# Optimization experiments

Measured on AMD Instinct MI355X. Metric: run time of the kernel, lower is better.

Reference implementation:

```python
import jax, jax.numpy as jnp
import numpy as np

K = 20  # kNN fan-out


def knn_idx(x, k):
    # x: (B, C, N). Negative squared pairwise distance; top-k largest = nearest.
    inner = -2.0 * jnp.einsum('bcn,bcm->bnm', x, x)        # (B, N, N)
    xx = jnp.sum(x * x, axis=1)                            # (B, N)
    pd = -xx[:, :, None] - inner - xx[:, None, :]          # (B, N, N)
    return jax.lax.top_k(pd, k)[1]                         # (B, N, k) int32


def get_graph_feature(x, k):
    # x: (B, C, N) -> edge features (B, 2C, N, k)
    idx = knn_idx(x, k)                                    # (B, N, k)
    xt = jnp.transpose(x, (0, 2, 1))                       # (B, N, C)
    nbrs = jax.vmap(lambda pts, ids: pts[ids])(xt, idx)    # (B, N, k, C)
    center = xt[:, :, None, :]                             # (B, N, 1, C)
    feat = jnp.concatenate(
        [nbrs - center, jnp.broadcast_to(center, nbrs.shape)], axis=-1)  # (B,N,k,2C)
    return jnp.transpose(feat, (0, 3, 1, 2))               # (B, 2C, N, k)


def vn_layer(W, x):
    # W: (out, in); x: (B, in, N, k) -> (B, out, N, k)
    return jnp.einsum('oi,bink->bonk', W, x)


def setup_inputs() -> dict:
    key = jax.random.key(0)
    ks = jax.random.split(key, 6)
    B, C, N = 16, 3, 2048
    num_classes = 10
    return {
        'x': jax.random.normal(ks[0], (B, C, N), dtype=jnp.float32),
        'W1': jax.random.normal(ks[1], (64, 6), dtype=jnp.float32),
        'W2': jax.random.normal(ks[2], (128, 64), dtype=jnp.float32),
        'W3': jax.random.normal(ks[3], (256, 128), dtype=jnp.float32),
        'fc_w': jax.random.normal(ks[4], (num_classes, 256), dtype=jnp.float32) * 0.0625,
        'fc_b': jax.random.normal(ks[5], (num_classes,), dtype=jnp.float32) * 0.0625,
    }


def reference(x, W1, W2, W3, fc_w, fc_b):
    h = get_graph_feature(x, K)          # (B, 6, N, k)
    h = vn_layer(W1, h)                  # (B, 64, N, k)
    h = jax.nn.relu(vn_layer(W2, h))     # (B, 128, N, k)
    h = jax.nn.relu(vn_layer(W3, h))     # (B, 256, N, k)
    h = jnp.max(h, axis=-1)              # max over neighbors k -> (B, 256, N)
    h = jnp.max(h, axis=-1)              # global max over points -> (B, 256)
    return h @ fc_w.T + fc_b             # (B, num_classes)
```

## Files before the change

### kernel.cpp

```cpp
#include <hip/hip_runtime.h>
#include <stdint.h>

typedef _Float16 v8h __attribute__((ext_vector_type(8)));
typedef _Float16 v2h __attribute__((ext_vector_type(2)));
typedef float v4f __attribute__((ext_vector_type(4)));
typedef float v16f __attribute__((ext_vector_type(16)));

#define NPTS 2048
#define BATCH 16
#define KNN 20
#define PAIRS (NPTS * KNN)

__device__ __forceinline__ unsigned pair_relu_h2(unsigned pu, unsigned qu) {
  v2h a = *(const v2h*)&pu;
  v2h b = *(const v2h*)&qu;
  v2h s = a + b;
  v2h z = {(_Float16)0.f, (_Float16)0.f};
  v2h r = __builtin_elementwise_max(s, z);
  return *(const unsigned*)&r;
}
__device__ __forceinline__ float fmax3(float a, float b, float c) {
  return fmaxf(fmaxf(a, b), c);
}

__global__ void prep_kernel(const float* __restrict__ W1, const float* __restrict__ W2,
                            float* __restrict__ M2a, float* __restrict__ M2b,
                            int* __restrict__ H) {
  if (blockIdx.x == 0 && threadIdx.x < 128) {
    int o = threadIdx.x;
    float a0 = 0, a1 = 0, a2 = 0, b0 = 0, b1 = 0, b2 = 0;
    for (int i = 0; i < 64; ++i) {
      float w2 = W2[o * 64 + i];
      const float* w1r = W1 + i * 6;
      a0 += w2 * w1r[0]; a1 += w2 * w1r[1]; a2 += w2 * w1r[2];
      b0 += w2 * (w1r[3] - w1r[0]); b1 += w2 * (w1r[4] - w1r[1]); b2 += w2 * (w1r[5] - w1r[2]);
    }
    M2a[o * 3 + 0] = a0; M2a[o * 3 + 1] = a1; M2a[o * 3 + 2] = a2;
    M2b[o * 3 + 0] = b0; M2b[o * 3 + 1] = b1; M2b[o * 3 + 2] = b2;
  }
  int g = blockIdx.x * 128 + threadIdx.x;
  if (g < BATCH * 256) H[g] = 0;
}

__global__ __launch_bounds__(64) void pq_kernel(const float* __restrict__ x,
                                                const float* __restrict__ M2a,
                                                const float* __restrict__ M2b,
                                                unsigned short* __restrict__ p,
                                                unsigned short* __restrict__ q) {
  int b = blockIdx.x >> 6;
  int j0 = (blockIdx.x & 63) << 5;
  int t = threadIdx.x;
  int o0 = t * 2;
  float a00 = M2a[o0 * 3 + 0], a01 = M2a[o0 * 3 + 1], a02 = M2a[o0 * 3 + 2];
  float a10 = M2a[o0 * 3 + 3], a11 = M2a[o0 * 3 + 4], a12 = M2a[o0 * 3 + 5];
  float b00 = M2b[o0 * 3 + 0], b01 = M2b[o0 * 3 + 1], b02 = M2b[o0 * 3 + 2];
  float b10 = M2b[o0 * 3 + 3], b11 = M2b[o0 * 3 + 4], b12 = M2b[o0 * 3 + 5];
  const float* xb = x + b * 3 * NPTS;
  unsigned* pw = (unsigned*)p;
  unsigned* qw = (unsigned*)q;
  for (int jj = 0; jj < 32; ++jj) {
    int j = j0 + jj;
    float x0 = xb[j], x1 = xb[NPTS + j], x2 = xb[2 * NPTS + j];
    float p0 = a00 * x0 + a01 * x1 + a02 * x2;
    float p1 = a10 * x0 + a11 * x1 + a12 * x2;
    float q0 = b00 * x0 + b01 * x1 + b02 * x2;
    float q1 = b10 * x0 + b11 * x1 + b12 * x2;
    size_t base = ((size_t)(b * NPTS + j)) * 64 + t;
    auto hp = __builtin_amdgcn_cvt_pkrtz(p0, p1);
    auto hq = __builtin_amdgcn_cvt_pkrtz(q0, q1);
    pw[base] = *(const unsigned*)&hp;
    qw[base] = *(const unsigned*)&hq;
  }
}

__global__ __launch_bounds__(512, 4) void knn_kernel(const float* __restrict__ x,
                                                     int* __restrict__ idxOut) {
  __shared__ float4 pts[NPTS];
  __shared__ unsigned long long cand[8][8][64];
  int b = blockIdx.x >> 5;
  int qblk = blockIdx.x & 31;
  const float* xb = x + b * 3 * NPTS;
  for (int i = threadIdx.x; i < NPTS; i += 512) {
    float X = xb[i], Y = xb[NPTS + i], Z = xb[2 * NPTS + i];
    pts[i] = make_float4(X, Y, Z, X * X + Y * Y + Z * Z);
  }
  __syncthreads();
  int wid = threadIdx.x >> 6, lane = threadIdx.x & 63;
  int qbase = qblk * 64 + wid * 8;

  float m2x[8], m2y[8], m2z[8], mn[8];
#pragma unroll
  for (int g = 0; g < 8; ++g) {
    float4 qp = pts[qbase + g];
    m2x[g] = -2.f * qp.x; m2y[g] = -2.f * qp.y; m2z[g] = -2.f * qp.z;
    mn[g] = 1e30f;
  }

  for (int s = 0; s < 32; ++s) {
    float4 P = pts[s * 64 + lane];
#pragma unroll
    for (int g = 0; g < 8; ++g) {
      float d = fmaf(m2x[g], P.x, fmaf(m2y[g], P.y, fmaf(m2z[g], P.z, P.w)));
      mn[g] = fminf(mn[g], d);
    }
  }

  float tau[8];
#pragma unroll
  for (int g = 0; g < 8; ++g) {
    float v = mn[g];
    for (int k = 2; k <= 64; k <<= 1) {
      for (int j = k >> 1; j > 0; j >>= 1) {
        float o = __shfl_xor(v, j);
        bool low = (lane & j) == 0;
        bool up = (lane & k) == 0;
        v = (low == up) ? fminf(v, o) : fmaxf(v, o);
      }
    }
    float t = __shfl(v, 19);
    tau[g] = t + fabsf(t) * 4e-6f + 1e-6f;
  }

  int cnt[8] = {0, 0, 0, 0, 0, 0, 0, 0};
  for (int s = 0; s < 32; ++s) {
    int i = s * 64 + lane;
    float4 P = pts[i];
#pragma unroll
    for (int g = 0; g < 8; ++g) {
      float d = fmaf(m2x[g], P.x, fmaf(m2y[g], P.y, fmaf(m2z[g], P.z, P.w)));
      bool take = d <= tau[g];
      unsigned long long mb = __ballot(take);
      if (take) {
        int pos = cnt[g] + __popcll(mb & ((1ull << lane) - 1ull));
        if (pos < 64) {
          unsigned kd = __float_as_uint(d + 64.f);
          cand[wid][g][pos] = (((unsigned long long)kd) << 32) | (unsigned)i;
        }
      }
      cnt[g] += __popcll(mb);
    }
  }

#pragma unroll
  for (int g = 0; g < 8; ++g) {
    int nc = cnt[g] < 64 ? cnt[g] : 64;
    unsigned long long k0 = (lane < nc) ? cand[wid][g][lane] : ~0ull;
    int r0 = 0;
    for (int i = 0; i < nc; ++i) r0 += (cand[wid][g][i] < k0) ? 1 : 0;
    long long obase = ((long long)b * NPTS + qbase + g) * KNN;
    if (lane < nc && r0 < KNN) idxOut[obase + r0] = (int)(k0 & 0xffffffffu);
  }
}

__global__ __launch_bounds__(256, 3) void gemm_max_kernel(
    const unsigned short* __restrict__ p, const unsigned short* __restrict__ q,
    const int* __restrict__ idx, const float* __restrict__ W3, int* __restrict__ H) {
  __shared__ __align__(16) unsigned short h2s[2][2][32 * 128];

  int b = blockIdx.x & 15;
  int w = blockIdx.x >> 4;
  int t = threadIdx.x;
  int lane = t & 63, wid = t >> 6;
  int col = lane & 31, hi = lane >> 5;

  v8h bfr0[8], bfr1[8];
#pragma unroll
  for (int kk = 0; kk < 8; ++kk) {
    const float* s0 = W3 + (size_t)(wid * 64 + col) * 128 + kk * 16 + hi * 8;
    const float* s1 = s0 + 32 * 128;
    v8h f0, f1;
#pragma unroll
    for (int jj = 0; jj < 8; ++jj) { f0[jj] = (_Float16)s0[jj]; f1[jj] = (_Float16)s1[jj]; }
    bfr0[kk] = f0; bfr1[kk] = f1;
  }

  const unsigned short* pB = p + (size_t)b * NPTS * 128;
  const unsigned short* qB = q + (size_t)b * NPTS * 128;
  const int* idxB = idx + (size_t)b * PAIRS;

  int pm = t >> 3;
  int c2 = t & 7;
  int st0 = pm * 128 + (((c2 * 2) ^ (pm & 7)) * 8);
  int st1 = pm * 128 + (((c2 * 2 + 1) ^ (pm & 7)) * 8);

  const int NT = PAIRS / 32;

  uint4 PA0, PA1, QA0, QA1, PB0, PB1, QB0, QB1;
  int jnA, jnB;
  {
    int prA = w * 32 + pm, prB = (w + 64) * 32 + pm;
    int jA = idxB[prA] & (NPTS - 1);
    int jB = idxB[prB] & (NPTS - 1);
    int nA = prA / 20, nB = prB / 20;
    PA0 = *(const uint4*)(pB + (size_t)jA * 128 + c2 * 16);
    PA1 = *(const uint4*)(pB + (size_t)jA * 128 + c2 * 16 + 8);
    QA0 = *(const uint4*)(qB + (size_t)nA * 128 + c2 * 16);
    QA1 = *(const uint4*)(qB + (size_t)nA * 128 + c2 * 16 + 8);
    PB0 = *(const uint4*)(pB + (size_t)jB * 128 + c2 * 16);
    PB1 = *(const uint4*)(pB + (size_t)jB * 128 + c2 * 16 + 8);
    QB0 = *(const uint4*)(qB + (size_t)nB * 128 + c2 * 16);
    QB1 = *(const uint4*)(qB + (size_t)nB * 128 + c2 * 16 + 8);
    jnA = idxB[(w + 128) * 32 + pm];
    jnB = idxB[(w + 192) * 32 + pm];
  }

  float vmx0 = 0.f, vmx1 = 0.f;
  int buf = 0;
  for (int T = w; T < NT; T += 128) {
    uint4 R;
    R.x = pair_relu_h2(PA0.x, QA0.x); R.y = pair_relu_h2(PA0.y, QA0.y);
    R.z = pair_relu_h2(PA0.z, QA0.z); R.w = pair_relu_h2(PA0.w, QA0.w);
    *(uint4*)&h2s[buf][0][st0] = R;
    R.x = pair_relu_h2(PA1.x, QA1.x); R.y = pair_relu_h2(PA1.y, QA1.y);
    R.z = pair_relu_h2(PA1.z, QA1.z); R.w = pair_relu_h2(PA1.w, QA1.w);
    *(uint4*)&h2s[buf][0][st1] = R;
    R.x = pair_relu_h2(PB0.x, QB0.x); R.y = pair_relu_h2(PB0.y, QB0.y);
    R.z = pair_relu_h2(PB0.z, QB0.z); R.w = pair_relu_h2(PB0.w, QB0.w);
    *(uint4*)&h2s[buf][1][st0] = R;
    R.x = pair_relu_h2(PB1.x, QB1.x); R.y = pair_relu_h2(PB1.y, QB1.y);
    R.z = pair_relu_h2(PB1.z, QB1.z); R.w = pair_relu_h2(PB1.w, QB1.w);
    *(uint4*)&h2s[buf][1][st1] = R;
    __syncthreads();

    int Tn = T + 128;
    if (Tn < NT) {
      int prA = Tn * 32 + pm, prB = (Tn + 64) * 32 + pm;
      int jA = jnA & (NPTS - 1), jB = jnB & (NPTS - 1);
      int nA = prA / 20, nB = prB / 20;
      PA0 = *(const uint4*)(pB + (size_t)jA * 128 + c2 * 16);
      PA1 = *(const uint4*)(pB + (size_t)jA * 128 + c2 * 16 + 8);
      QA0 = *(const uint4*)(qB + (size_t)nA * 128 + c2 * 16);
      QA1 = *(const uint4*)(qB + (size_t)nA * 128 + c2 * 16 + 8);
      PB0 = *(const uint4*)(pB + (size_t)jB * 128 + c2 * 16);
      PB1 = *(const uint4*)(pB + (size_t)jB * 128 + c2 * 16 + 8);
      QB0 = *(const uint4*)(qB + (size_t)nB * 128 + c2 * 16);
      QB1 = *(const uint4*)(qB + (size_t)nB * 128 + c2 * 16 + 8);
      int T2 = T + 256;
      if (T2 < NT) {
        jnA = idxB[T2 * 32 + pm];
        jnB = idxB[(T2 + 64) * 32 + pm];
      }
    }

    {
      v16f acc0 = {0.f}, acc1 = {0.f};
#pragma unroll
      for (int kk = 0; kk < 8; ++kk) {
        v8h a = *(const v8h*)&h2s[buf][0][col * 128 + (((kk * 2 + hi) ^ (col & 7)) * 8)];
        acc0 = __builtin_amdgcn_mfma_f32_32x32x16_f16(a, bfr0[kk], acc0, 0, 0, 0);
        acc1 = __builtin_amdgcn_mfma_f32_32x32x16_f16(a, bfr1[kk], acc1, 0, 0, 0);
      }
      float m0 = fmax3(acc0[0], acc0[1], acc0[2]);
      float m1 = fmax3(acc0[3], acc0[4], acc0[5]);
      float m2 = fmax3(acc0[6], acc0[7], acc0[8]);
      float m3 = fmax3(acc0[9], acc0[10], acc0[11]);
      float m4 = fmax3(acc0[12], acc0[13], acc0[14]);
      vmx0 = fmax3(fmax3(m0, m1, m2), fmax3(m3, m4, acc0[15]), vmx0);
      float n0 = fmax3(acc1[0], acc1[1], acc1[2]);
      float n1 = fmax3(acc1[3], acc1[4], acc1[5]);
      float n2 = fmax3(acc1[6], acc1[7], acc1[8]);
      float n3 = fmax3(acc1[9], acc1[10], acc1[11]);
      float n4 = fmax3(acc1[12], acc1[13], acc1[14]);
      vmx1 = fmax3(fmax3(n0, n1, n2), fmax3(n3, n4, acc1[15]), vmx1);
    }
    {
      v16f acc0 = {0.f}, acc1 = {0.f};
#pragma unroll
      for (int kk = 0; kk < 8; ++kk) {
        v8h a = *(const v8h*)&h2s[buf][1][col * 128 + (((kk * 2 + hi) ^ (col & 7)) * 8)];
        acc0 = __builtin_amdgcn_mfma_f32_32x32x16_f16(a, bfr0[kk], acc0, 0, 0, 0);
        acc1 = __builtin_amdgcn_mfma_f32_32x32x16_f16(a, bfr1[kk], acc1, 0, 0, 0);
      }
      float m0 = fmax3(acc0[0], acc0[1], acc0[2]);
      float m1 = fmax3(acc0[3], acc0[4], acc0[5]);
      float m2 = fmax3(acc0[6], acc0[7], acc0[8]);
      float m3 = fmax3(acc0[9], acc0[10], acc0[11]);
      float m4 = fmax3(acc0[12], acc0[13], acc0[14]);
      vmx0 = fmax3(fmax3(m0, m1, m2), fmax3(m3, m4, acc0[15]), vmx0);
      float n0 = fmax3(acc1[0], acc1[1], acc1[2]);
      float n1 = fmax3(acc1[3], acc1[4], acc1[5]);
      float n2 = fmax3(acc1[6], acc1[7], acc1[8]);
      float n3 = fmax3(acc1[9], acc1[10], acc1[11]);
      float n4 = fmax3(acc1[12], acc1[13], acc1[14]);
      vmx1 = fmax3(fmax3(n0, n1, n2), fmax3(n3, n4, acc1[15]), vmx1);
    }
    buf ^= 1;
  }

  float v0 = fmaxf(vmx0, __shfl_xor(vmx0, 32));
  float v1 = fmaxf(vmx1, __shfl_xor(vmx1, 32));
  if (hi == 0) {
    atomicMax(&H[b * 256 + wid * 64 + col], __float_as_int(v0));
    atomicMax(&H[b * 256 + wid * 64 + 32 + col], __float_as_int(v1));
  }
}

__global__ __launch_bounds__(64) void fc_kernel(const int* __restrict__ Hi,
                                                const float* __restrict__ fcw,
                                                const float* __restrict__ fcb,
                                                float* __restrict__ out) {
  int b = blockIdx.x / 10, r = blockIdx.x % 10;
  int lane = threadIdx.x;
  const float* Hb = (const float*)Hi + b * 256;
  float s = 0.f;
#pragma unroll
  for (int c = lane; c < 256; c += 64) s += Hb[c] * fcw[r * 256 + c];
#pragma unroll
  for (int m = 32; m > 0; m >>= 1) s += __shfl_xor(s, m);
  if (lane == 0) out[b * 10 + r] = s + fcb[r];
}

extern "C" void kernel_launch(void* const* d_in, const int* in_sizes, int n_in,
                              void* d_out, int out_size, void* d_ws, size_t ws_size,
                              hipStream_t stream) {
  const float* x   = (const float*)d_in[0];
  const float* W1  = (const float*)d_in[1];
  const float* W2  = (const float*)d_in[2];
  const float* W3  = (const float*)d_in[3];
  const float* fcw = (const float*)d_in[4];
  const float* fcb = (const float*)d_in[5];
  float* out = (float*)d_out;
  char* ws = (char*)d_ws;

  float* M2a = (float*)(ws + 0);
  float* M2b = (float*)(ws + 1536);
  int* H     = (int*)(ws + 4096);
  int* idx   = (int*)(ws + 24576);
  unsigned short* p = (unsigned short*)(ws + 3145728);
  unsigned short* q = (unsigned short*)(ws + 12582912);

  prep_kernel<<<32, 128, 0, stream>>>(W1, W2, M2a, M2b, H);
  pq_kernel<<<BATCH * 64, 64, 0, stream>>>(x, M2a, M2b, p, q);
  knn_kernel<<<BATCH * 32, 512, 0, stream>>>(x, idx);
  gemm_max_kernel<<<BATCH * 64, 256, 0, stream>>>(p, q, idx, W3, H);
  fc_kernel<<<BATCH * 10, 64, 0, stream>>>(H, fcw, fcb, out);
}
```

Measured before the change: 162.1 us.

## Fold weight prep, H zeroing and p/q projection into the kNN kernel

```diff
diff --git a/kernel.cpp b/kernel.cpp
--- a/kernel.cpp
+++ b/kernel.cpp
@@ -23,70 +23,65 @@
   return fmaxf(fmaxf(a, b), c);
 }
 
-__global__ void prep_kernel(const float* __restrict__ W1, const float* __restrict__ W2,
-                            float* __restrict__ M2a, float* __restrict__ M2b,
-                            int* __restrict__ H) {
-  if (blockIdx.x == 0 && threadIdx.x < 128) {
-    int o = threadIdx.x;
-    float a0 = 0, a1 = 0, a2 = 0, b0 = 0, b1 = 0, b2 = 0;
-    for (int i = 0; i < 64; ++i) {
-      float w2 = W2[o * 64 + i];
-      const float* w1r = W1 + i * 6;
-      a0 += w2 * w1r[0]; a1 += w2 * w1r[1]; a2 += w2 * w1r[2];
-      b0 += w2 * (w1r[3] - w1r[0]); b1 += w2 * (w1r[4] - w1r[1]); b2 += w2 * (w1r[5] - w1r[2]);
-    }
-    M2a[o * 3 + 0] = a0; M2a[o * 3 + 1] = a1; M2a[o * 3 + 2] = a2;
-    M2b[o * 3 + 0] = b0; M2b[o * 3 + 1] = b1; M2b[o * 3 + 2] = b2;
-  }
-  int g = blockIdx.x * 128 + threadIdx.x;
-  if (g < BATCH * 256) H[g] = 0;
-}
-
-__global__ __launch_bounds__(64) void pq_kernel(const float* __restrict__ x,
-                                                const float* __restrict__ M2a,
-                                                const float* __restrict__ M2b,
-                                                unsigned short* __restrict__ p,
-                                                unsigned short* __restrict__ q) {
-  int b = blockIdx.x >> 6;
-  int j0 = (blockIdx.x & 63) << 5;
-  int t = threadIdx.x;
-  int o0 = t * 2;
-  float a00 = M2a[o0 * 3 + 0], a01 = M2a[o0 * 3 + 1], a02 = M2a[o0 * 3 + 2];
-  float a10 = M2a[o0 * 3 + 3], a11 = M2a[o0 * 3 + 4], a12 = M2a[o0 * 3 + 5];
-  float b00 = M2b[o0 * 3 + 0], b01 = M2b[o0 * 3 + 1], b02 = M2b[o0 * 3 + 2];
-  float b10 = M2b[o0 * 3 + 3], b11 = M2b[o0 * 3 + 4], b12 = M2b[o0 * 3 + 5];
-  const float* xb = x + b * 3 * NPTS;
-  unsigned* pw = (unsigned*)p;
-  unsigned* qw = (unsigned*)q;
-  for (int jj = 0; jj < 32; ++jj) {
-    int j = j0 + jj;
-    float x0 = xb[j], x1 = xb[NPTS + j], x2 = xb[2 * NPTS + j];
-    float p0 = a00 * x0 + a01 * x1 + a02 * x2;
-    float p1 = a10 * x0 + a11 * x1 + a12 * x2;
-    float q0 = b00 * x0 + b01 * x1 + b02 * x2;
-    float q1 = b10 * x0 + b11 * x1 + b12 * x2;
-    size_t base = ((size_t)(b * NPTS + j)) * 64 + t;
-    auto hp = __builtin_amdgcn_cvt_pkrtz(p0, p1);
-    auto hq = __builtin_amdgcn_cvt_pkrtz(q0, q1);
-    pw[base] = *(const unsigned*)&hp;
-    qw[base] = *(const unsigned*)&hq;
-  }
-}
-
-__global__ __launch_bounds__(512, 4) void knn_kernel(const float* __restrict__ x,
-                                                     int* __restrict__ idxOut) {
+__global__ __launch_bounds__(512, 2) void knn_kernel(
+    const float* __restrict__ x, int* __restrict__ idxOut,
+    const float* __restrict__ W1, const float* __restrict__ W2,
+    unsigned short* __restrict__ p, unsigned short* __restrict__ q,
+    int* __restrict__ H) {
   __shared__ float4 pts[NPTS];
   __shared__ unsigned long long cand[8][8][64];
   int b = blockIdx.x >> 5;
   int qblk = blockIdx.x & 31;
   const float* xb = x + b * 3 * NPTS;
+
+  if (qblk == 0 && threadIdx.x < 256) H[b * 256 + threadIdx.x] = 0;
+
   for (int i = threadIdx.x; i < NPTS; i += 512) {
     float X = xb[i], Y = xb[NPTS + i], Z = xb[2 * NPTS + i];
     pts[i] = make_float4(X, Y, Z, X * X + Y * Y + Z * Z);
   }
+
+  int wid = threadIdx.x >> 6, lane = threadIdx.x & 63;
+
+  float a0 = 0, a1 = 0, a2 = 0, a3 = 0, a4 = 0, a5 = 0;
+  float c0 = 0, c1 = 0, c2 = 0, c3 = 0, c4 = 0, c5 = 0;
+  {
+    int o0 = lane * 2;
+    const float* w2a = W2 + o0 * 64;
+    const float* w2b = w2a + 64;
+    for (int i = 0; i < 64; ++i) {
+      const float* w1r = W1 + i * 6;
+      float u0 = w1r[0], u1 = w1r[1], u2 = w1r[2];
+      float v0 = w1r[3] - u0, v1 = w1r[4] - u1, v2 = w1r[5] - u2;
+      float wA = w2a[i], wB = w2b[i];
+      a0 += wA * u0; a1 += wA * u1; a2 += wA * u2;
+      a3 += wA * v0; a4 += wA * v1; a5 += wA * v2;
+      c0 += wB * u0; c1 += wB * u1; c2 += wB * u2;
+      c3 += wB * v0; c4 += wB * v1; c5 += wB * v2;
+    }
+  }
   __syncthreads();
-  int wid = threadIdx.x >> 6, lane = threadIdx.x & 63;
+
   int qbase = qblk * 64 + wid * 8;
+
+  {
+    unsigned* pw = (unsigned*)p;
+    unsigned* qw = (unsigned*)q;
+#pragma unroll
+    for (int g = 0; g < 8; ++g) {
+      int j = qbase + g;
+      float4 qp = pts[j];
+      float p0 = a0 * qp.x + a1 * qp.y + a2 * qp.z;
+      float p1 = c0 * qp.x + c1 * qp.y + c2 * qp.z;
+      float q0 = a3 * qp.x + a4 * qp.y + a5 * qp.z;
+      float q1 = c3 * qp.x + c4 * qp.y + c5 * qp.z;
+      size_t base = ((size_t)(b * NPTS + j)) * 64 + lane;
+      auto hp = __builtin_amdgcn_cvt_pkrtz(p0, p1);
+      auto hq = __builtin_amdgcn_cvt_pkrtz(q0, q1);
+      pw[base] = *(const unsigned*)&hp;
+      qw[base] = *(const unsigned*)&hq;
+    }
+  }
 
   float m2x[8], m2y[8], m2z[8], mn[8];
 #pragma unroll
@@ -322,16 +317,12 @@
   float* out = (float*)d_out;
   char* ws = (char*)d_ws;
 
-  float* M2a = (float*)(ws + 0);
-  float* M2b = (float*)(ws + 1536);
   int* H     = (int*)(ws + 4096);
   int* idx   = (int*)(ws + 24576);
   unsigned short* p = (unsigned short*)(ws + 3145728);
   unsigned short* q = (unsigned short*)(ws + 12582912);
 
-  prep_kernel<<<32, 128, 0, stream>>>(W1, W2, M2a, M2b, H);
-  pq_kernel<<<BATCH * 64, 64, 0, stream>>>(x, M2a, M2b, p, q);
-  knn_kernel<<<BATCH * 32, 512, 0, stream>>>(x, idx);
+  knn_kernel<<<BATCH * 32, 512, 0, stream>>>(x, idx, W1, W2, p, q, H);
   gemm_max_kernel<<<BATCH * 64, 256, 0, stream>>>(p, q, idx, W3, H);
   fc_kernel<<<BATCH * 10, 64, 0, stream>>>(H, fcw, fcb, out);
 }
```

Result: slower. 168.0 us (+3.7%).
